# Optimization experiments

Hardware: AMD Instinct MI355X
Metric: run time of the kernel (lower is better)

## Reference

```python
import jax, jax.numpy as jnp
import numpy as np

D_MODEL = 1024
N_BLOCKS = 4
D_STATE = 16
D_CONV = 4
EXPAND = 2
DT_RANK = 64  # ceil(1024/16)
D_INNER = EXPAND * D_MODEL
BATCH = 2
SEQLEN = 1024


def setup_inputs() -> dict:
    key = jax.random.key(0)
    ks = jax.random.split(key, 8)
    s = 0.02
    f = lambda k, sh: (jax.random.normal(k, sh, dtype=jnp.float32) * s)
    return {
        "x": jax.random.normal(ks[0], (BATCH, SEQLEN, D_MODEL), dtype=jnp.float32),
        "norm_w": jnp.ones((N_BLOCKS, D_MODEL), jnp.float32),
        "norm_b": jnp.zeros((N_BLOCKS, D_MODEL), jnp.float32),
        "in_proj_w": f(ks[1], (N_BLOCKS, D_MODEL, 2 * D_INNER)),
        "conv_w": f(ks[2], (N_BLOCKS, D_INNER, D_CONV)),
        "conv_b": jnp.zeros((N_BLOCKS, D_INNER), jnp.float32),
        "xproj_w": f(ks[3], (N_BLOCKS, D_INNER, DT_RANK + 2 * D_STATE)),
        "dtproj_w": f(ks[4], (N_BLOCKS, DT_RANK, D_INNER)),
        "dtproj_b": jnp.full((N_BLOCKS, D_INNER), -4.6, jnp.float32),  # softplus ~ 0.01
        "A_log": jnp.tile(jnp.log(jnp.arange(1, D_STATE + 1, dtype=jnp.float32))[None, None, :], (N_BLOCKS, D_INNER, 1)),
        "skip_D": jnp.ones((N_BLOCKS, D_INNER), jnp.float32),
        "out_proj_w": f(ks[5], (N_BLOCKS, D_INNER, D_MODEL)),
        "fn_w": jnp.ones((D_MODEL,), jnp.float32),
        "fn_b": jnp.zeros((D_MODEL,), jnp.float32),
    }


def _layer_norm(x, w, b):
    m = jnp.mean(x, -1, keepdims=True)
    v = jnp.mean((x - m) ** 2, -1, keepdims=True)
    return (x - m) * jax.lax.rsqrt(v + 1e-5) * w + b


def _selective_scan(u, dt, A, Bm, Cm, Dp):
    # u, dt: (B,L,E)  A: (E,N)  Bm, Cm: (B,L,N)  Dp: (E,)
    dA = jnp.exp(dt[..., None] * A)                 # (B,L,E,N) ZOH discretization of A
    dBu = (dt * u)[..., None] * Bm[:, :, None, :]   # (B,L,E,N) Euler discretization of B*u

    def step(h, inp):
        dA_t, dBu_t, C_t = inp
        h = dA_t * h + dBu_t                        # (B,E,N)
        y = jnp.einsum('ben,bn->be', h, C_t)
        return h, y

    h0 = jnp.zeros((u.shape[0], u.shape[2], A.shape[1]), u.dtype)
    xs = (jnp.moveaxis(dA, 1, 0), jnp.moveaxis(dBu, 1, 0), jnp.moveaxis(Cm, 1, 0))
    _, ys = jax.lax.scan(step, h0, xs)
    y = jnp.moveaxis(ys, 0, 1)                      # (B,L,E)
    return y + u * Dp


def _mamba(x, in_w, cw, cb, xw, dtw, dtb, A_log, Dp, ow):
    L = x.shape[1]
    xz = x @ in_w                                   # (B,L,2E)
    u, z = jnp.split(xz, 2, axis=-1)
    K = cw.shape[1]
    up = jnp.pad(u, ((0, 0), (K - 1, 0), (0, 0)))   # causal depthwise conv
    conv = cb + sum(up[:, k:k + L, :] * cw[:, k] for k in range(K))
    u = jax.nn.silu(conv)
    dbl = u @ xw                                    # (B,L,R+2N)
    dt = jax.nn.softplus(dbl[..., :DT_RANK] @ dtw + dtb)
    Bm = dbl[..., DT_RANK:DT_RANK + D_STATE]
    Cm = dbl[..., DT_RANK + D_STATE:]
    A = -jnp.exp(A_log)
    y = _selective_scan(u, dt, A, Bm, Cm, Dp)
    y = y * jax.nn.silu(z)                          # gating branch
    return y @ ow


def _forward(x, norm_w, norm_b, in_proj_w, conv_w, conv_b, xproj_w, dtproj_w, dtproj_b, A_log, skip_D, out_proj_w, fn_w, fn_b):
    for i in range(N_BLOCKS):
        h = _layer_norm(x, norm_w[i], norm_b[i])
        h = _mamba(h, in_proj_w[i], conv_w[i], conv_b[i], xproj_w[i], dtproj_w[i], dtproj_b[i], A_log[i], skip_D[i], out_proj_w[i])
        x = x + h                                   # pre-norm residual
    return _layer_norm(x, fn_w, fn_b)


def reference(x, norm_w, norm_b, in_proj_w, conv_w, conv_b, xproj_w, dtproj_w, dtproj_b, A_log, skip_D, out_proj_w, fn_w, fn_b):
    return _forward(x, norm_w, norm_b, in_proj_w, conv_w, conv_b, xproj_w, dtproj_w, dtproj_b, A_log, skip_D, out_proj_w, fn_w, fn_b)
```

## Files before the change

### kernel.cpp

```cpp
#include <hip/hip_runtime.h>
#include <hip/hip_bf16.h>
#include <math.h>

#define BATCH 2
#define SEQLEN 1024
#define DMODEL 1024
#define DINNER 2048
#define DSTATE 16
#define DTRANK 64
#define XDIM 96
#define KCONV 4
#define NBLOCKS 4
#define MROWS (BATCH*SEQLEN)

#define NCHUNK 32
#define CLEN (SEQLEN/NCHUNK)
#define SUN 4

typedef short bf16x8 __attribute__((ext_vector_type(8)));
typedef unsigned short u16x8 __attribute__((ext_vector_type(8)));
typedef float f32x4 __attribute__((ext_vector_type(4)));

__device__ __forceinline__ unsigned short f2bf(float x) {
    union { float f; unsigned u; } c; c.f = x;
    unsigned r = c.u + 0x7FFFu + ((c.u >> 16) & 1u);
    return (unsigned short)(r >> 16);
}
__device__ __forceinline__ float bf2f(unsigned short h) {
    union { unsigned u; float f; } c; c.u = (unsigned)h << 16;
    return c.f;
}

__device__ __forceinline__ void gload16(const void* src, void* dst) {
    __builtin_amdgcn_global_load_lds(
        (const __attribute__((address_space(1))) void*)src,
        (__attribute__((address_space(3))) void*)dst, 16, 0, 0);
}

__global__ __launch_bounds__(256) void lnc_k(const float* __restrict__ x,
    const float* __restrict__ w, const float* __restrict__ b,
    float* __restrict__ resid, unsigned short* __restrict__ out)
{
    int row = blockIdx.x;
    int tid = threadIdx.x;
    size_t off = (size_t)row * DMODEL + tid * 4;
    float4 v = *(const float4*)(x + off);
    *(float4*)(resid + off) = v;
    float s  = v.x + v.y + v.z + v.w;
    float sq = v.x*v.x + v.y*v.y + v.z*v.z + v.w*v.w;
    #pragma unroll
    for (int o = 32; o > 0; o >>= 1) {
        s  += __shfl_down(s, o);
        sq += __shfl_down(sq, o);
    }
    __shared__ float ss[4], sq4[4];
    int wid = tid >> 6;
    if ((tid & 63) == 0) { ss[wid] = s; sq4[wid] = sq; }
    __syncthreads();
    if (tid == 0) {
        ss[0]  = ss[0] + ss[1] + ss[2] + ss[3];
        sq4[0] = sq4[0] + sq4[1] + sq4[2] + sq4[3];
    }
    __syncthreads();
    float mean = ss[0] * (1.0f / DMODEL);
    float var  = sq4[0] * (1.0f / DMODEL) - mean * mean;
    float rstd = rsqrtf(var + 1e-5f);
    float4 wv = *(const float4*)(w + tid * 4);
    float4 bv = *(const float4*)(b + tid * 4);
    ushort4 h;
    h.x = f2bf((v.x - mean) * rstd * wv.x + bv.x);
    h.y = f2bf((v.y - mean) * rstd * wv.y + bv.y);
    h.z = f2bf((v.z - mean) * rstd * wv.z + bv.z);
    h.w = f2bf((v.w - mean) * rstd * wv.w + bv.w);
    *(ushort4*)(out + off) = h;
}

template<int FINAL>
__global__ __launch_bounds__(256) void predln_k(
    const float* __restrict__ pout, float* __restrict__ resid,
    const float* __restrict__ w, const float* __restrict__ b,
    unsigned short* __restrict__ hb16, float* __restrict__ fout)
{
    int row = blockIdx.x;
    int tid = threadIdx.x;
    const size_t MN = (size_t)MROWS * DMODEL;
    size_t off = (size_t)row * DMODEL + tid * 4;
    float4 p0 = *(const float4*)(pout + off);
    float4 p1 = *(const float4*)(pout + off + MN);
    float4 p2 = *(const float4*)(pout + off + 2 * MN);
    float4 p3 = *(const float4*)(pout + off + 3 * MN);
    float4 r  = *(const float4*)(resid + off);
    float4 v;
    v.x = r.x + (p0.x + p1.x) + (p2.x + p3.x);
    v.y = r.y + (p0.y + p1.y) + (p2.y + p3.y);
    v.z = r.z + (p0.z + p1.z) + (p2.z + p3.z);
    v.w = r.w + (p0.w + p1.w) + (p2.w + p3.w);
    if (!FINAL) *(float4*)(resid + off) = v;

    float s  = v.x + v.y + v.z + v.w;
    float sq = v.x*v.x + v.y*v.y + v.z*v.z + v.w*v.w;
    #pragma unroll
    for (int o = 32; o > 0; o >>= 1) {
        s  += __shfl_down(s, o);
        sq += __shfl_down(sq, o);
    }
    __shared__ float ss[4], sq4[4];
    int wid = tid >> 6;
    if ((tid & 63) == 0) { ss[wid] = s; sq4[wid] = sq; }
    __syncthreads();
    if (tid == 0) {
        ss[0]  = ss[0] + ss[1] + ss[2] + ss[3];
        sq4[0] = sq4[0] + sq4[1] + sq4[2] + sq4[3];
    }
    __syncthreads();
    float mean = ss[0] * (1.0f / DMODEL);
    float var  = sq4[0] * (1.0f / DMODEL) - mean * mean;
    float rstd = rsqrtf(var + 1e-5f);
    float4 wv = *(const float4*)(w + tid * 4);
    float4 bv = *(const float4*)(b + tid * 4);
    float o0 = (v.x - mean) * rstd * wv.x + bv.x;
    float o1 = (v.y - mean) * rstd * wv.y + bv.y;
    float o2 = (v.z - mean) * rstd * wv.z + bv.z;
    float o3 = (v.w - mean) * rstd * wv.w + bv.w;
    if (FINAL) {
        *(float4*)(fout + off) = make_float4(o0, o1, o2, o3);
    } else {
        ushort4 h;
        h.x = f2bf(o0); h.y = f2bf(o1); h.z = f2bf(o2); h.w = f2bf(o3);
        *(ushort4*)(hb16 + off) = h;
    }
}

__global__ __launch_bounds__(256) void wtr2_k(
    const float* __restrict__ W, unsigned short* __restrict__ WT,
    int N, int K, long long wstride, long long wtstride)
{
    const float* Wl = W + (size_t)blockIdx.z * wstride;
    unsigned short* WTl = WT + (size_t)blockIdx.z * wtstride;
    __shared__ float T[64][65];
    int n0 = blockIdx.x * 64, k0 = blockIdx.y * 64;
    int tid = threadIdx.x;
    int kk = tid >> 4, nn = (tid & 15) * 4;
    #pragma unroll
    for (int p = 0; p < 4; ++p) {
        float4 v = make_float4(0.f, 0.f, 0.f, 0.f);
        if (n0 + nn + 4 <= N)
            v = *(const float4*)(Wl + (size_t)(k0 + p * 16 + kk) * N + n0 + nn);
        T[p * 16 + kk][nn + 0] = v.x;
        T[p * 16 + kk][nn + 1] = v.y;
        T[p * 16 + kk][nn + 2] = v.z;
        T[p * 16 + kk][nn + 3] = v.w;
    }
    __syncthreads();
    int n2 = tid >> 4, k2 = (tid & 15) * 4;
    #pragma unroll
    for (int p = 0; p < 4; ++p) {
        int nrow = n0 + p * 16 + n2;
        ushort4 h = {0, 0, 0, 0};
        if (nrow < N) {
            h.x = f2bf(T[k2 + 0][p * 16 + n2]);
            h.y = f2bf(T[k2 + 1][p * 16 + n2]);
            h.z = f2bf(T[k2 + 2][p * 16 + n2]);
            h.w = f2bf(T[k2 + 3][p * 16 + n2]);
        }
        *(ushort4*)(WTl + (size_t)nrow * K + k0 + k2) = h;
    }
}

template<int EPI, int BN, int SWZX = 0, int SWZY = 0>
__global__ __launch_bounds__(256) void mgemm6_k(
    const unsigned short* __restrict__ A,
    const unsigned short* __restrict__ BT,
    float* __restrict__ out0, float* __restrict__ out1,
    const float* __restrict__ bias,
    int N, int Kf, int Kloc)
{
    constexpr int WN = BN / 2;
    constexpr int NJ = WN / 16;
    __shared__ unsigned short As[3][128 * 32];
    __shared__ unsigned short Bs[3][BN * 32];
    int tid = threadIdx.x;
    int lane = tid & 63, w = tid >> 6;
    int wr = w >> 1, wc = w & 1;
    int bxx = blockIdx.x, byy = blockIdx.y;
    if constexpr (SWZX > 0) {
        constexpr int TOT = SWZX * SWZY;
        int f = bxx + SWZX * byy;
        int nf = (f & 7) * (TOT / 8) + (f >> 3);
        bxx = nf % SWZX; byy = nf / SWZX;
    }
    int m0 = byy * 128, n0 = bxx * BN;
    int lr = lane & 15, G = lane >> 4;

    int ra0 = w * 32 + (lane >> 2);
    int ra1 = ra0 + 16;
    int ga0 = (lane & 3) ^ ((ra0 >> 1) & 3);
    int ga1 = (lane & 3) ^ ((ra1 >> 1) & 3);
    int rb0 = w * (BN / 4) + (lane >> 2);
    int gb0 = (lane & 3) ^ ((rb0 >> 1) & 3);
    int rb1 = rb0 + 16;
    int gb1 = (lane & 3) ^ ((rb1 >> 1) & 3);

    int kz = blockIdx.z * Kloc;
    const unsigned short* pa0 = A  + (size_t)(m0 + ra0) * Kf + kz + ga0 * 8;
    const unsigned short* pa1 = A  + (size_t)(m0 + ra1) * Kf + kz + ga1 * 8;
    const unsigned short* pb0 = BT + (size_t)(n0 + rb0) * Kf + kz + gb0 * 8;
    const unsigned short* pb1 = BT + (size_t)(n0 + rb1) * Kf + kz + gb1 * 8;
    int dA0 = (w * 32) * 32, dA1 = dA0 + 16 * 32;
    int dB0 = (w * (BN / 4)) * 32, dB1 = dB0 + 16 * 32;

#define ISSUE(tt, bufi) do {                                   \
        gload16(pa0 + (tt) * 32, &As[bufi][dA0]);              \
        gload16(pa1 + (tt) * 32, &As[bufi][dA1]);              \
        gload16(pb0 + (tt) * 32, &Bs[bufi][dB0]);              \
        if (BN == 128) gload16(pb1 + (tt) * 32, &Bs[bufi][dB1]); \
    } while (0)

    f32x4 acc[4][NJ] = {};
    int T = Kloc / 32;

    ISSUE(0, 0);
    if (T > 1) ISSUE(1, 1);

    int cur = 0;
    for (int t = 0; t < T; ++t) {
        if (t + 1 < T) {
            if constexpr (BN == 128)
                asm volatile("s_waitcnt vmcnt(4)" ::: "memory");
            else
                asm volatile("s_waitcnt vmcnt(3)" ::: "memory");
        } else {
            asm volatile("s_waitcnt vmcnt(0)" ::: "memory");
        }
        __builtin_amdgcn_s_barrier();
        if (t + 2 < T) {
            int nb = cur + 2; if (nb >= 3) nb -= 3;
            ISSUE(t + 2, nb);
        }
        bf16x8 af[4], bfr[NJ];
        #pragma unroll
        for (int i = 0; i < 4; ++i) {
            int r = wr * 64 + i * 16 + lr;
            af[i] = *(const bf16x8*)&As[cur][r * 32 + ((G ^ ((r >> 1) & 3)) << 3)];
        }
        #pragma unroll
        for (int j = 0; j < NJ; ++j) {
            int r = wc * WN + j * 16 + lr;
            bfr[j] = *(const bf16x8*)&Bs[cur][r * 32 + ((G ^ ((r >> 1) & 3)) << 3)];
        }
        #pragma unroll
        for (int i = 0; i < 4; ++i)
            #pragma unroll
            for (int j = 0; j < NJ; ++j)
                acc[i][j] = __builtin_amdgcn_mfma_f32_16x16x32_bf16(
                    af[i], bfr[j], acc[i][j], 0, 0, 0);
        __builtin_amdgcn_s_barrier();
        cur = (cur + 1 == 3) ? 0 : cur + 1;
    }
#undef ISSUE

    int rbase = m0 + wr * 64 + (lane >> 4) * 4;
    int cbase = n0 + wc * WN + lr;
    #pragma unroll
    for (int i = 0; i < 4; ++i)
        #pragma unroll
        for (int j = 0; j < NJ; ++j)
            #pragma unroll
            for (int r = 0; r < 4; ++r) {
                int row = rbase + i * 16 + r;
                int col = cbase + j * 16;
                float c = acc[i][j][r];
                if (EPI == 2) {
                    out0[(size_t)blockIdx.z * MROWS * N + (size_t)row * N + col] = c;
                } else if (EPI == 3) {
                    if (col < XDIM)
                        out0[(size_t)blockIdx.z * MROWS * XDIM +
                             (size_t)row * XDIM + col] = c;
                } else {
                    float cc = c + bias[col];
                    cc = fmaxf(cc, 0.f) + log1pf(__expf(-fabsf(cc)));
                    ((unsigned short*)out0)[(size_t)row * N + col] = f2bf(cc);
                }
            }
}

template<int EPI, int SWZX = 0, int SWZY = 0>
__global__ __launch_bounds__(512) void mgemm8_k(
    const unsigned short* __restrict__ A,
    const unsigned short* __restrict__ BT,
    float* __restrict__ out0, float* __restrict__ out1,
    int N, int Kf, int Kloc)
{
    __shared__ unsigned short As[3][256 * 32];
    __shared__ unsigned short Bs[3][128 * 32];
    int tid = threadIdx.x;
    int lane = tid & 63, w = tid >> 6;
    int wr = w >> 1, wc = w & 1;
    int bxx = blockIdx.x, byy = blockIdx.y;
    if constexpr (SWZX > 0) {
        constexpr int TOT = SWZX * SWZY;
        int f = bxx + SWZX * byy;
        int nf = (f & 7) * (TOT / 8) + (f >> 3);
        bxx = nf % SWZX; byy = nf / SWZX;
    }
    int m0 = byy * 256, n0 = bxx * 128;
    int lr = lane & 15, G = lane >> 4;

    int ra0 = w * 32 + (lane >> 2);
    int ra1 = ra0 + 16;
    int ga0 = (lane & 3) ^ ((ra0 >> 1) & 3);
    int ga1 = (lane & 3) ^ ((ra1 >> 1) & 3);
    int rb0 = w * 16 + (lane >> 2);
    int gb0 = (lane & 3) ^ ((rb0 >> 1) & 3);

    int kz = blockIdx.z * Kloc;
    const unsigned short* pa0 = A  + (size_t)(m0 + ra0) * Kf + kz + ga0 * 8;
    const unsigned short* pa1 = A  + (size_t)(m0 + ra1) * Kf + kz + ga1 * 8;
    const unsigned short* pb0 = BT + (size_t)(n0 + rb0) * Kf + kz + gb0 * 8;
    int dA0 = (w * 32) * 32, dA1 = dA0 + 16 * 32;
    int dB0 = (w * 16) * 32;

#define ISSUE8(tt, bufi) do {                                  \
        gload16(pa0 + (tt) * 32, &As[bufi][dA0]);              \
        gload16(pa1 + (tt) * 32, &As[bufi][dA1]);              \
        gload16(pb0 + (tt) * 32, &Bs[bufi][dB0]);              \
    } while (0)

    f32x4 acc[4][4] = {};
    int T = Kloc / 32;

    ISSUE8(0, 0);
    if (T > 1) ISSUE8(1, 1);

    int cur = 0;
    for (int t = 0; t < T; ++t) {
        if (t + 1 < T)
            asm volatile("s_waitcnt vmcnt(3)" ::: "memory");
        else
            asm volatile("s_waitcnt vmcnt(0)" ::: "memory");
        __builtin_amdgcn_s_barrier();
        if (t + 2 < T) {
            int nb = cur + 2; if (nb >= 3) nb -= 3;
            ISSUE8(t + 2, nb);
        }
        bf16x8 af[4], bfr[4];
        #pragma unroll
        for (int i = 0; i < 4; ++i) {
            int r = wr * 64 + i * 16 + lr;
            af[i] = *(const bf16x8*)&As[cur][r * 32 + ((G ^ ((r >> 1) & 3)) << 3)];
        }
        #pragma unroll
        for (int j = 0; j < 4; ++j) {
            int r = wc * 64 + j * 16 + lr;
            bfr[j] = *(const bf16x8*)&Bs[cur][r * 32 + ((G ^ ((r >> 1) & 3)) << 3)];
        }
        #pragma unroll
        for (int i = 0; i < 4; ++i)
            #pragma unroll
            for (int j = 0; j < 4; ++j)
                acc[i][j] = __builtin_amdgcn_mfma_f32_16x16x32_bf16(
                    af[i], bfr[j], acc[i][j], 0, 0, 0);
        __builtin_amdgcn_s_barrier();
        cur = (cur + 1 == 3) ? 0 : cur + 1;
    }
#undef ISSUE8

    int rbase = m0 + wr * 64 + (lane >> 4) * 4;
    int cbase = n0 + wc * 64 + lr;
    #pragma unroll
    for (int i = 0; i < 4; ++i)
        #pragma unroll
        for (int j = 0; j < 4; ++j)
            #pragma unroll
            for (int r = 0; r < 4; ++r) {
                int row = rbase + i * 16 + r;
                int col = cbase + j * 16;
                float c = acc[i][j][r];
                if (EPI == 0) {
                    if (col < DINNER)
                        ((unsigned short*)out0)[(size_t)row * DINNER + col] = f2bf(c);
                    else
                        ((unsigned short*)out1)[(size_t)row * DINNER + (col - DINNER)] = f2bf(c);
                } else {
                    out0[(size_t)blockIdx.z * MROWS * N + (size_t)row * N + col] = c;
                }
            }
}

#define XSPLIT 16
__global__ __launch_bounds__(256) void xprojR_k(
    const float* __restrict__ part, float* __restrict__ dbl,
    unsigned short* __restrict__ db64)
{
    int idx = blockIdx.x * 256 + threadIdx.x;
    float s = 0.f;
    #pragma unroll
    for (int k = 0; k < XSPLIT; ++k)
        s += part[(size_t)k * MROWS * XDIM + idx];
    dbl[idx] = s;
    int col = idx % XDIM;
    if (col < DTRANK)
        db64[(size_t)(idx / XDIM) * DTRANK + col] = f2bf(s);
}

__global__ __launch_bounds__(256) void conv_k(const unsigned short* __restrict__ u,
    const float* __restrict__ cw, const float* __restrict__ cb,
    unsigned short* __restrict__ out)
{
    int idx = blockIdx.x * 256 + threadIdx.x;
    int c8 = idx & (DINNER / 8 - 1);
    int t  = (idx >> 8) & (SEQLEN - 1);
    int b  = idx >> 18;
    int e0 = c8 * 8;
    size_t base = (size_t)b * SEQLEN * DINNER + (size_t)t * DINNER + e0;
    u16x8 rows[KCONV];
    #pragma unroll
    for (int k = 0; k < KCONV; ++k) {
        int tt = t + k - (KCONV - 1);
        u16x8 zv = {0,0,0,0,0,0,0,0};
        rows[k] = (tt >= 0) ?
            *(const u16x8*)(u + base + (size_t)(k - (KCONV - 1)) * DINNER) : zv;
    }
    u16x8 o;
    #pragma unroll
    for (int j = 0; j < 8; ++j) {
        float4 wv = *(const float4*)(cw + (size_t)(e0 + j) * KCONV);
        float acc = cb[e0 + j];
        acc = fmaf(bf2f(rows[0][j]), wv.x, acc);
        acc = fmaf(bf2f(rows[1][j]), wv.y, acc);
        acc = fmaf(bf2f(rows[2][j]), wv.z, acc);
        acc = fmaf(bf2f(rows[3][j]), wv.w, acc);
        o[j] = f2bf(acc / (1.f + __expf(-acc)));
    }
    *(u16x8*)(out + base) = o;
}

template<int CTRL>
__device__ __forceinline__ float qadd(float x) {
    int y = __builtin_amdgcn_update_dpp(0, __float_as_int(x), CTRL, 0xF, 0xF, true);
    return x + __int_as_float(y);
}

__global__ __launch_bounds__(512) void scan_k(
    const unsigned short* __restrict__ dt, const unsigned short* __restrict__ uc,
    const float* __restrict__ dbl, const unsigned short* __restrict__ z,
    const float* __restrict__ A_log, const float* __restrict__ Dp,
    unsigned short* __restrict__ yout)
{
    __shared__ float sAlo[NCHUNK][8][2][4], sAhi[NCHUNK][8][2][4];
    __shared__ float sBlo[NCHUNK][8][2][4], sBhi[NCHUNK][8][2][4];
    int tid = threadIdx.x;
    int sub = tid & 1;
    int ei  = (tid >> 1) & 7;
    int ch  = tid >> 4;
    int bid = blockIdx.x;
    int blk = (bid & 7) * 64 + (bid >> 3);
    int eg  = blk & 255;
    int b   = blk >> 8;
    int e   = eg * 8 + ei;

    const float L2E = 1.4426950408889634f;
    float AstL2[8];
    {
        const float* ap = A_log + (size_t)e * DSTATE + sub * 8;
        #pragma unroll
        for (int q = 0; q < 2; ++q) {
            float4 v = *(const float4*)(ap + q * 4);
            AstL2[q * 4 + 0] = -__expf(v.x) * L2E;
            AstL2[q * 4 + 1] = -__expf(v.y) * L2E;
            AstL2[q * 4 + 2] = -__expf(v.z) * L2E;
            AstL2[q * 4 + 3] = -__expf(v.w) * L2E;
        }
    }
    size_t base_e = (size_t)b * SEQLEN * DINNER + e;
    size_t base_x = (size_t)b * SEQLEN * XDIM + DTRANK + sub * 8;
    int t0c = ch * CLEN;

    float h[8] = {0.f, 0.f, 0.f, 0.f, 0.f, 0.f, 0.f, 0.f};
    float ssum = 0.f;
    for (int t0 = t0c; t0 < t0c + CLEN; t0 += SUN) {
        float sdt[SUN], su[SUN];
        #pragma unroll
        for (int u = 0; u < SUN; ++u) {
            size_t te = base_e + (size_t)(t0 + u) * DINNER;
            sdt[u] = bf2f(dt[te]);
            su[u]  = bf2f(uc[te]);
        }
        #pragma unroll
        for (int u = 0; u < SUN; ++u) {
            const float* dx = dbl + base_x + (size_t)(t0 + u) * XDIM;
            float4 bn0 = *(const float4*)(dx);
            float4 bn1 = *(const float4*)(dx + 4);
            float dtu = sdt[u] * su[u];
            ssum += sdt[u];
            h[0] = fmaf(__builtin_amdgcn_exp2f(sdt[u] * AstL2[0]), h[0], dtu * bn0.x);
            h[1] = fmaf(__builtin_amdgcn_exp2f(sdt[u] * AstL2[1]), h[1], dtu * bn0.y);
            h[2] = fmaf(__builtin_amdgcn_exp2f(sdt[u] * AstL2[2]), h[2], dtu * bn0.z);
            h[3] = fmaf(__builtin_amdgcn_exp2f(sdt[u] * AstL2[3]), h[3], dtu * bn0.w);
            h[4] = fmaf(__builtin_amdgcn_exp2f(sdt[u] * AstL2[4]), h[4], dtu * bn1.x);
            h[5] = fmaf(__builtin_amdgcn_exp2f(sdt[u] * AstL2[5]), h[5], dtu * bn1.y);
            h[6] = fmaf(__builtin_amdgcn_exp2f(sdt[u] * AstL2[6]), h[6], dtu * bn1.z);
            h[7] = fmaf(__builtin_amdgcn_exp2f(sdt[u] * AstL2[7]), h[7], dtu * bn1.w);
        }
    }
    float a_[8];
    #pragma unroll
    for (int i = 0; i < 8; ++i) a_[i] = __builtin_amdgcn_exp2f(AstL2[i] * ssum);
    *(f32x4*)&sAlo[ch][ei][sub][0] = *(f32x4*)&a_[0];
    *(f32x4*)&sAhi[ch][ei][sub][0] = *(f32x4*)&a_[4];
    *(f32x4*)&sBlo[ch][ei][sub][0] = *(f32x4*)&h[0];
    *(f32x4*)&sBhi[ch][ei][sub][0] = *(f32x4*)&h[4];
    __syncthreads();

    #pragma unroll
    for (int s = 1; s < NCHUNK; s <<= 1) {
        float pa[8], pb[8];
        bool act = (ch >= s);
        if (act) {
            *(f32x4*)&pa[0] = *(const f32x4*)&sAlo[ch - s][ei][sub][0];
            *(f32x4*)&pa[4] = *(const f32x4*)&sAhi[ch - s][ei][sub][0];
            *(f32x4*)&pb[0] = *(const f32x4*)&sBlo[ch - s][ei][sub][0];
            *(f32x4*)&pb[4] = *(const f32x4*)&sBhi[ch - s][ei][sub][0];
        }
        __syncthreads();
        if (act) {
            #pragma unroll
            for (int i = 0; i < 8; ++i) {
                h[i]  = fmaf(a_[i], pb[i], h[i]);
                a_[i] *= pa[i];
            }
            *(f32x4*)&sAlo[ch][ei][sub][0] = *(f32x4*)&a_[0];
            *(f32x4*)&sAhi[ch][ei][sub][0] = *(f32x4*)&a_[4];
            *(f32x4*)&sBlo[ch][ei][sub][0] = *(f32x4*)&h[0];
            *(f32x4*)&sBhi[ch][ei][sub][0] = *(f32x4*)&h[4];
        }
        __syncthreads();
    }

    if (ch > 0) {
        *(f32x4*)&h[0] = *(const f32x4*)&sBlo[ch - 1][ei][sub][0];
        *(f32x4*)&h[4] = *(const f32x4*)&sBhi[ch - 1][ei][sub][0];
    } else {
        #pragma unroll
        for (int i = 0; i < 8; ++i) h[i] = 0.f;
    }

    float Dk = Dp[e];
    for (int t0 = t0c; t0 < t0c + CLEN; t0 += SUN) {
        float sdt[SUN], su[SUN], zz[SUN];
        #pragma unroll
        for (int u = 0; u < SUN; ++u) {
            size_t te = base_e + (size_t)(t0 + u) * DINNER;
            sdt[u] = bf2f(dt[te]);
            su[u]  = bf2f(uc[te]);
            zz[u]  = bf2f(z[te]);
        }
        #pragma unroll
        for (int u = 0; u < SUN; ++u) {
            const float* dx = dbl + base_x + (size_t)(t0 + u) * XDIM;
            float4 bn0 = *(const float4*)(dx);
            float4 bn1 = *(const float4*)(dx + 4);
            float4 cn0 = *(const float4*)(dx + 16);
            float4 cn1 = *(const float4*)(dx + 20);
            float dtu = sdt[u] * su[u];
            h[0] = fmaf(__builtin_amdgcn_exp2f(sdt[u] * AstL2[0]), h[0], dtu * bn0.x);
            h[1] = fmaf(__builtin_amdgcn_exp2f(sdt[u] * AstL2[1]), h[1], dtu * bn0.y);
            h[2] = fmaf(__builtin_amdgcn_exp2f(sdt[u] * AstL2[2]), h[2], dtu * bn0.z);
            h[3] = fmaf(__builtin_amdgcn_exp2f(sdt[u] * AstL2[3]), h[3], dtu * bn0.w);
            h[4] = fmaf(__builtin_amdgcn_exp2f(sdt[u] * AstL2[4]), h[4], dtu * bn1.x);
            h[5] = fmaf(__builtin_amdgcn_exp2f(sdt[u] * AstL2[5]), h[5], dtu * bn1.y);
            h[6] = fmaf(__builtin_amdgcn_exp2f(sdt[u] * AstL2[6]), h[6], dtu * bn1.z);
            h[7] = fmaf(__builtin_amdgcn_exp2f(sdt[u] * AstL2[7]), h[7], dtu * bn1.w);
            float p = h[0] * cn0.x + h[1] * cn0.y + h[2] * cn0.z + h[3] * cn0.w
                    + h[4] * cn1.x + h[5] * cn1.y + h[6] * cn1.z + h[7] * cn1.w;
            p = qadd<0xB1>(p);
            if (sub == 0) {
                float zvv = zz[u];
                float yv = p + su[u] * Dk;
                yout[base_e + (size_t)(t0 + u) * DINNER] =
                    f2bf(yv * (zvv / (1.f + __expf(-zvv))));
            }
        }
    }
}

extern "C" void kernel_launch(void* const* d_in, const int* in_sizes, int n_in,
                              void* d_out, int out_size, void* d_ws, size_t ws_size,
                              hipStream_t stream)
{
    const float* x         = (const float*)d_in[0];
    const float* norm_w    = (const float*)d_in[1];
    const float* norm_b    = (const float*)d_in[2];
    const float* in_proj_w = (const float*)d_in[3];
    const float* conv_w    = (const float*)d_in[4];
    const float* conv_b    = (const float*)d_in[5];
    const float* xproj_w   = (const float*)d_in[6];
    const float* dtproj_w  = (const float*)d_in[7];
    const float* dtproj_b  = (const float*)d_in[8];
    const float* A_log     = (const float*)d_in[9];
    const float* skip_D    = (const float*)d_in[10];
    const float* out_proj_w= (const float*)d_in[11];
    const float* fn_w      = (const float*)d_in[12];
    const float* fn_b      = (const float*)d_in[13];

    float* resid = (float*)d_out;
    float* ws    = (float*)d_ws;
    const size_t M1 = 1024 * 1024;
    unsigned short* wtib = (unsigned short*)(ws);
    unsigned short* wtob = (unsigned short*)(ws + 8  * M1);
    unsigned short* wtxp = (unsigned short*)(ws + 12 * M1);
    unsigned short* wtdt = (unsigned short*)(ws + 12 * M1 + M1 / 2);
    unsigned short* hb16 = (unsigned short*)(ws + 13 * M1);
    unsigned short* ub16 = (unsigned short*)(ws + 14 * M1);
    unsigned short* zb16 = (unsigned short*)(ws + 16 * M1);
    unsigned short* ucb16= (unsigned short*)(ws + 18 * M1);
    unsigned short* dtb16= (unsigned short*)(ws + 20 * M1);
    float*          dblb = ws + 22 * M1;
    unsigned short* db64 = (unsigned short*)(ws + 22 * M1 + M1 / 4);
    unsigned short* yb16 = (unsigned short*)(ws + 23 * M1);
    float*          xpart= ws + 25 * M1;
    float*          pout = ws + 28 * M1;

    wtr2_k<<<dim3(2 * DINNER / 64, DMODEL / 64, NBLOCKS), 256, 0, stream>>>(
        in_proj_w, wtib, 2 * DINNER, DMODEL,
        (long long)DMODEL * 2 * DINNER, (long long)2 * DINNER * DMODEL);
    wtr2_k<<<dim3(DMODEL / 64, DINNER / 64, NBLOCKS), 256, 0, stream>>>(
        out_proj_w, wtob, DMODEL, DINNER,
        (long long)DINNER * DMODEL, (long long)DMODEL * DINNER);
    wtr2_k<<<dim3(2, DINNER / 64, NBLOCKS), 256, 0, stream>>>(
        xproj_w, wtxp, XDIM, DINNER,
        (long long)DINNER * XDIM, (long long)128 * DINNER);
    wtr2_k<<<dim3(DINNER / 64, 1, NBLOCKS), 256, 0, stream>>>(
        dtproj_w, wtdt, DINNER, DTRANK,
        (long long)DTRANK * DINNER, (long long)DINNER * DTRANK);

    lnc_k<<<MROWS, 256, 0, stream>>>(x, norm_w, norm_b, resid, hb16);

    for (int i = 0; i < NBLOCKS; ++i) {
        mgemm8_k<0, 32, 8><<<dim3(2 * DINNER / 128, MROWS / 256, 1), 512, 0, stream>>>(
            hb16, wtib + (size_t)i * 2 * DINNER * DMODEL,
            (float*)ub16, (float*)zb16, 2 * DINNER, DMODEL, DMODEL);
        conv_k<<<(MROWS * DINNER / 8) / 256, 256, 0, stream>>>(
            ub16, conv_w + (size_t)i * DINNER * KCONV,
            conv_b + (size_t)i * DINNER, ucb16);
        mgemm6_k<3, 128><<<dim3(1, MROWS / 128, XSPLIT), 256, 0, stream>>>(
            ucb16, wtxp + (size_t)i * 128 * DINNER,
            xpart, nullptr, nullptr, XDIM, DINNER, DINNER / XSPLIT);
        xprojR_k<<<(MROWS * XDIM) / 256, 256, 0, stream>>>(xpart, dblb, db64);
        mgemm6_k<4, 64><<<dim3(DINNER / 64, MROWS / 128, 1), 256, 0, stream>>>(
            db64, wtdt + (size_t)i * DINNER * DTRANK,
            (float*)dtb16, nullptr, dtproj_b + (size_t)i * DINNER,
            DINNER, DTRANK, DTRANK);
        scan_k<<<BATCH * DINNER / 8, 512, 0, stream>>>(
            dtb16, ucb16, dblb, zb16,
            A_log + (size_t)i * DINNER * DSTATE, skip_D + (size_t)i * DINNER, yb16);
        mgemm8_k<2, 8, 8><<<dim3(DMODEL / 128, MROWS / 256, 4), 512, 0, stream>>>(
            yb16, wtob + (size_t)i * DMODEL * DINNER,
            pout, nullptr, DMODEL, DINNER, DINNER / 4);
        if (i < NBLOCKS - 1)
            predln_k<0><<<MROWS, 256, 0, stream>>>(pout, resid,
                norm_w + (i + 1) * DMODEL, norm_b + (i + 1) * DMODEL,
                hb16, nullptr);
        else
            predln_k<1><<<MROWS, 256, 0, stream>>>(pout, resid,
                fn_w, fn_b, nullptr, resid);
    }
}
```

Before: 594.5 us.

## Use 32x32x16 MFMA with 128x128 tiles and 256-thread blocks for projections

Replaces the 256x128-tile, 512-thread GEMM used for the in and out projections with a 128x128-tile, 256-thread kernel. Each wave now computes 64x64 using 32x32x16 bf16 MFMA instructions instead of 16x16x32 ones, with a new fragment layout and epilogue indexing. The smaller tile doubles the grid and halves LDS per block, which may raise occupancy and wave count. The trade-off is lower arithmetic reuse per block, and the LDS read pattern changes for the new fragment shape.

```diff
diff --git a/kernel.cpp b/kernel.cpp
--- a/kernel.cpp
+++ b/kernel.cpp
@@ -20,6 +20,7 @@
 typedef short bf16x8 __attribute__((ext_vector_type(8)));
 typedef unsigned short u16x8 __attribute__((ext_vector_type(8)));
 typedef float f32x4 __attribute__((ext_vector_type(4)));
+typedef float f32x16 __attribute__((ext_vector_type(16)));
 
 __device__ __forceinline__ unsigned short f2bf(float x) {
     union { float f; unsigned u; } c; c.f = x;
@@ -285,13 +286,13 @@
 }
 
 template<int EPI, int SWZX = 0, int SWZY = 0>
-__global__ __launch_bounds__(512) void mgemm8_k(
+__global__ __launch_bounds__(256) void mgemm7_k(
     const unsigned short* __restrict__ A,
     const unsigned short* __restrict__ BT,
     float* __restrict__ out0, float* __restrict__ out1,
     int N, int Kf, int Kloc)
 {
-    __shared__ unsigned short As[3][256 * 32];
+    __shared__ unsigned short As[3][128 * 32];
     __shared__ unsigned short Bs[3][128 * 32];
     int tid = threadIdx.x;
     int lane = tid & 63, w = tid >> 6;
@@ -303,78 +304,92 @@
         int nf = (f & 7) * (TOT / 8) + (f >> 3);
         bxx = nf % SWZX; byy = nf / SWZX;
     }
-    int m0 = byy * 256, n0 = bxx * 128;
-    int lr = lane & 15, G = lane >> 4;
+    int m0 = byy * 128, n0 = bxx * 128;
+    int l31 = lane & 31, hb = lane >> 5;
 
     int ra0 = w * 32 + (lane >> 2);
     int ra1 = ra0 + 16;
     int ga0 = (lane & 3) ^ ((ra0 >> 1) & 3);
     int ga1 = (lane & 3) ^ ((ra1 >> 1) & 3);
-    int rb0 = w * 16 + (lane >> 2);
+    int rb0 = w * 32 + (lane >> 2);
     int gb0 = (lane & 3) ^ ((rb0 >> 1) & 3);
+    int rb1 = rb0 + 16;
+    int gb1 = (lane & 3) ^ ((rb1 >> 1) & 3);
 
     int kz = blockIdx.z * Kloc;
     const unsigned short* pa0 = A  + (size_t)(m0 + ra0) * Kf + kz + ga0 * 8;
     const unsigned short* pa1 = A  + (size_t)(m0 + ra1) * Kf + kz + ga1 * 8;
     const unsigned short* pb0 = BT + (size_t)(n0 + rb0) * Kf + kz + gb0 * 8;
+    const unsigned short* pb1 = BT + (size_t)(n0 + rb1) * Kf + kz + gb1 * 8;
     int dA0 = (w * 32) * 32, dA1 = dA0 + 16 * 32;
-    int dB0 = (w * 16) * 32;
-
-#define ISSUE8(tt, bufi) do {                                  \
+    int dB0 = (w * 32) * 32, dB1 = dB0 + 16 * 32;
+
+#define ISSUE7(tt, bufi) do {                                  \
         gload16(pa0 + (tt) * 32, &As[bufi][dA0]);              \
         gload16(pa1 + (tt) * 32, &As[bufi][dA1]);              \
         gload16(pb0 + (tt) * 32, &Bs[bufi][dB0]);              \
+        gload16(pb1 + (tt) * 32, &Bs[bufi][dB1]);              \
     } while (0)
 
-    f32x4 acc[4][4] = {};
+    f32x16 acc[2][2] = {};
     int T = Kloc / 32;
 
-    ISSUE8(0, 0);
-    if (T > 1) ISSUE8(1, 1);
+    ISSUE7(0, 0);
+    if (T > 1) ISSUE7(1, 1);
 
     int cur = 0;
     for (int t = 0; t < T; ++t) {
         if (t + 1 < T)
-            asm volatile("s_waitcnt vmcnt(3)" ::: "memory");
+            asm volatile("s_waitcnt vmcnt(4)" ::: "memory");
         else
             asm volatile("s_waitcnt vmcnt(0)" ::: "memory");
         __builtin_amdgcn_s_barrier();
         if (t + 2 < T) {
             int nb = cur + 2; if (nb >= 3) nb -= 3;
-            ISSUE8(t + 2, nb);
-        }
-        bf16x8 af[4], bfr[4];
-        #pragma unroll
-        for (int i = 0; i < 4; ++i) {
-            int r = wr * 64 + i * 16 + lr;
-            af[i] = *(const bf16x8*)&As[cur][r * 32 + ((G ^ ((r >> 1) & 3)) << 3)];
-        }
-        #pragma unroll
-        for (int j = 0; j < 4; ++j) {
-            int r = wc * 64 + j * 16 + lr;
-            bfr[j] = *(const bf16x8*)&Bs[cur][r * 32 + ((G ^ ((r >> 1) & 3)) << 3)];
-        }
-        #pragma unroll
-        for (int i = 0; i < 4; ++i)
+            ISSUE7(t + 2, nb);
+        }
+        bf16x8 af[2][2], bfr[2][2];
+        #pragma unroll
+        for (int i = 0; i < 2; ++i) {
+            int r = wr * 64 + i * 32 + l31;
+            int sw = (r >> 1) & 3;
             #pragma unroll
-            for (int j = 0; j < 4; ++j)
-                acc[i][j] = __builtin_amdgcn_mfma_f32_16x16x32_bf16(
-                    af[i], bfr[j], acc[i][j], 0, 0, 0);
+            for (int s = 0; s < 2; ++s) {
+                int g = s * 2 + hb;
+                af[i][s] = *(const bf16x8*)&As[cur][r * 32 + ((g ^ sw) << 3)];
+            }
+        }
+        #pragma unroll
+        for (int j = 0; j < 2; ++j) {
+            int r = wc * 64 + j * 32 + l31;
+            int sw = (r >> 1) & 3;
+            #pragma unroll
+            for (int s = 0; s < 2; ++s) {
+                int g = s * 2 + hb;
+                bfr[j][s] = *(const bf16x8*)&Bs[cur][r * 32 + ((g ^ sw) << 3)];
+            }
+        }
+        #pragma unroll
+        for (int i = 0; i < 2; ++i)
+            #pragma unroll
+            for (int j = 0; j < 2; ++j)
+                #pragma unroll
+                for (int s = 0; s < 2; ++s)
+                    acc[i][j] = __builtin_amdgcn_mfma_f32_32x32x16_bf16(
+                        af[i][s], bfr[j][s], acc[i][j], 0, 0, 0);
         __builtin_amdgcn_s_barrier();
         cur = (cur + 1 == 3) ? 0 : cur + 1;
     }
-#undef ISSUE8
-
-    int rbase = m0 + wr * 64 + (lane >> 4) * 4;
-    int cbase = n0 + wc * 64 + lr;
-    #pragma unroll
-    for (int i = 0; i < 4; ++i)
-        #pragma unroll
-        for (int j = 0; j < 4; ++j)
+#undef ISSUE7
+
+    #pragma unroll
+    for (int i = 0; i < 2; ++i)
+        #pragma unroll
+        for (int j = 0; j < 2; ++j)
             #pragma unroll
-            for (int r = 0; r < 4; ++r) {
-                int row = rbase + i * 16 + r;
-                int col = cbase + j * 16;
+            for (int r = 0; r < 16; ++r) {
+                int row = m0 + wr * 64 + i * 32 + (r & 3) + 8 * (r >> 2) + 4 * hb;
+                int col = n0 + wc * 64 + j * 32 + l31;
                 float c = acc[i][j][r];
                 if (EPI == 0) {
                     if (col < DINNER)
@@ -637,7 +652,7 @@
     lnc_k<<<MROWS, 256, 0, stream>>>(x, norm_w, norm_b, resid, hb16);
 
     for (int i = 0; i < NBLOCKS; ++i) {
-        mgemm8_k<0, 32, 8><<<dim3(2 * DINNER / 128, MROWS / 256, 1), 512, 0, stream>>>(
+        mgemm7_k<0, 32, 16><<<dim3(2 * DINNER / 128, MROWS / 128, 1), 256, 0, stream>>>(
             hb16, wtib + (size_t)i * 2 * DINNER * DMODEL,
             (float*)ub16, (float*)zb16, 2 * DINNER, DMODEL, DMODEL);
         conv_k<<<(MROWS * DINNER / 8) / 256, 256, 0, stream>>>(
@@ -654,7 +669,7 @@
         scan_k<<<BATCH * DINNER / 8, 512, 0, stream>>>(
             dtb16, ucb16, dblb, zb16,
             A_log + (size_t)i * DINNER * DSTATE, skip_D + (size_t)i * DINNER, yb16);
-        mgemm8_k<2, 8, 8><<<dim3(DMODEL / 128, MROWS / 256, 4), 512, 0, stream>>>(
+        mgemm7_k<2, 8, 16><<<dim3(DMODEL / 128, MROWS / 128, 4), 256, 0, stream>>>(
             yb16, wtob + (size_t)i * DMODEL * DINNER,
             pout, nullptr, DMODEL, DINNER, DINNER / 4);
         if (i < NBLOCKS - 1)
```

Result: faster. 575.7 us (-3.2%).
